# Performance work log

Measured on AMD Instinct MI355X. Metric: run time of the kernel, lower is better.

Reference implementation:

```python
import jax, jax.numpy as jnp
import numpy as np

NUM_NODES = 50000
NUM_EDGES = 600000
NUM_FEAT = 128
HIDDEN = 512
N_OUT = 128
K = 3
N_GRAPHS = 128


def setup_inputs() -> dict:
    key = jax.random.key(0)
    ks = jax.random.split(key, 12)
    feature = jax.random.normal(ks[0], (NUM_NODES, NUM_FEAT), dtype=jnp.float32)
    edge_index = jax.random.randint(ks[1], (2, NUM_EDGES), 0, NUM_NODES, dtype=jnp.int64)
    protein_batch = jnp.sort(jax.random.randint(ks[2], (NUM_NODES,), 0, N_GRAPHS, dtype=jnp.int64))
    s = 0.05
    # ChebConv weights stored [K, in, out] (x @ W), single shared bias per conv
    W1 = jax.random.normal(ks[3], (K, NUM_FEAT, NUM_FEAT), dtype=jnp.float32) * s
    b1 = jax.random.normal(ks[4], (NUM_FEAT,), dtype=jnp.float32) * s
    W2 = jax.random.normal(ks[5], (K, NUM_FEAT, 2 * NUM_FEAT), dtype=jnp.float32) * s
    b2 = jax.random.normal(ks[6], (2 * NUM_FEAT,), dtype=jnp.float32) * s
    fc1_w = jax.random.normal(ks[7], (3 * NUM_FEAT, HIDDEN), dtype=jnp.float32) * s
    fc1_b = jax.random.normal(ks[8], (HIDDEN,), dtype=jnp.float32) * s
    fc2_w = jax.random.normal(ks[9], (HIDDEN, N_OUT), dtype=jnp.float32) * s
    fc2_b = jax.random.normal(ks[10], (N_OUT,), dtype=jnp.float32) * s
    return {"feature": feature, "edge_index": edge_index, "protein_batch": protein_batch,
            "W1": W1, "b1": b1, "W2": W2, "b2": b2,
            "fc1_w": fc1_w, "fc1_b": fc1_b, "fc2_w": fc2_w, "fc2_b": fc2_b}


def _cheb_conv(x, src, dst, edge_w, W, b):
    # PyG ChebConv with sym normalization, lambda_max=2 => scaled Laplacian
    # L_hat has zero diagonal and off-diag weights -1/sqrt(d_i d_j) (edge_w).
    def prop(h):
        return jax.ops.segment_sum(edge_w[:, None] * h[src], dst, num_segments=NUM_NODES)

    Tx0 = x
    out = Tx0 @ W[0]
    Tx1 = prop(x)
    out = out + Tx1 @ W[1]
    for k in range(2, W.shape[0]):
        Tx2 = 2.0 * prop(Tx1) - Tx0
        out = out + Tx2 @ W[k]
        Tx0, Tx1 = Tx1, Tx2
    return out + b


def reference(feature, edge_index, protein_batch, W1, b1, W2, b2, fc1_w, fc1_b, fc2_w, fc2_b):
    src, dst = edge_index[0], edge_index[1]
    deg = jax.ops.segment_sum(jnp.ones_like(src, dtype=feature.dtype), src, num_segments=NUM_NODES)
    dinv = jnp.where(deg > 0, jax.lax.rsqrt(jnp.maximum(deg, 1.0)), 0.0)
    edge_w = -dinv[src] * dinv[dst]  # (2/lambda_max)*L_sym off-diagonal; diag cancels to 0

    gx = jax.nn.relu(_cheb_conv(feature, src, dst, edge_w, W1, b1))
    gx = jax.nn.relu(_cheb_conv(gx, src, dst, edge_w, W2, b2))
    gx = jnp.concatenate([gx, feature], axis=1)  # [N, 3*F]

    # global_mean_pool
    sums = jax.ops.segment_sum(gx, protein_batch, num_segments=N_GRAPHS)
    cnts = jax.ops.segment_sum(jnp.ones((gx.shape[0],), gx.dtype), protein_batch, num_segments=N_GRAPHS)
    pooled = sums / jnp.maximum(cnts, 1.0)[:, None]

    h = jax.nn.relu(pooled @ fc1_w + fc1_b)  # dropout is identity in eval
    return h @ fc2_w + fc2_b
```

## Files before the change

### kernel.cpp

```cpp
#include <hip/hip_runtime.h>
#include <hip/hip_bf16.h>

#define NNODES 50000
#define NEDGES 600000
#define NB 196

typedef short vs8 __attribute__((ext_vector_type(8)));
typedef float floatx4 __attribute__((ext_vector_type(4)));

__device__ __forceinline__ float us2f(unsigned short u) {
    unsigned int x = ((unsigned int)u) << 16;
    float f;
    __builtin_memcpy(&f, &x, 4);
    return f;
}
__device__ __forceinline__ unsigned short f2us(float f) {
    unsigned int x;
    __builtin_memcpy(&x, &f, 4);
    unsigned int r = x + 0x7fffu + ((x >> 16) & 1u);
    return (unsigned short)(r >> 16);
}
__device__ __forceinline__ float ldf(const void* p, int i, int ff) {
    if (ff) return us2f(((const unsigned short*)p)[i]);
    return ((const float*)p)[i];
}
__device__ __forceinline__ int2 ldnt_sw(const int2* p) {
    unsigned long long v =
        __builtin_nontemporal_load(reinterpret_cast<const unsigned long long*>(p));
    int2 r;
    r.x = (int)(unsigned int)(v & 0xffffffffULL);
    r.y = (int)(unsigned int)(v >> 32);
    return r;
}

__global__ void k_detect(const int* ei, const unsigned int* fw, int* iflag, int* fflag) {
    int lane = threadIdx.x;
    int odd1 = ei[2 * lane + 1];
    int odd2 = ei[128 + 2 * lane + 1];
    unsigned long long nz = __ballot(odd1 != 0 || odd2 != 0);
    unsigned int e = (fw[lane] >> 7) & 0xffu;
    unsigned long long h = __ballot(e > 100u && e < 160u);
    if (lane == 0) {
        *iflag = (nz == 0ULL) ? 1 : 0;
        *fflag = (__popcll(h) > 40) ? 1 : 0;
    }
}

__global__ void k_init(const int* pb, const int* iflag, int* deg, int* indeg,
                       int* b32, float* psum) {
    int i = blockIdx.x * 256 + threadIdx.x;
    if (i < NNODES) {
        deg[i] = 0;
        indeg[i] = 0;
        int f = *iflag;
        b32[i] = pb[((size_t)i) << f];
    }
    if (i < 128 * 384) psum[i] = 0.f;
}

__global__ void k_degree(const int* ei, const int* iflag, int* deg, int* indeg,
                         int* rank) {
    int e = blockIdx.x * blockDim.x + threadIdx.x;
    if (e >= NEDGES) return;
    int f = *iflag;
    int s = ei[((size_t)e) << f];
    int d = ei[((size_t)(NEDGES + e)) << f];
    atomicAdd(&deg[s], 1);
    int r = atomicAdd(&indeg[d], 1);
    rank[e] = r;
}

__global__ void k_scan1(const int* indeg, const int* deg, int* bsum, float* dinv) {
    __shared__ int sh[256];
    int t = threadIdx.x;
    int i = blockIdx.x * 256 + t;
    int v = (i < NNODES) ? indeg[i] : 0;
    if (i < NNODES) {
        int d = deg[i];
        dinv[i] = d > 0 ? rsqrtf((float)d) : 0.f;
    }
    sh[t] = v;
    __syncthreads();
    for (int off = 128; off > 0; off >>= 1) {
        if (t < off) sh[t] += sh[t + off];
        __syncthreads();
    }
    if (t == 0) bsum[blockIdx.x] = sh[0];
}

__global__ void k_scan2(const int* bsum, int* boff, int* rowptr,
                        const int* batch32, int* pcnt) {
    __shared__ int sh[256];
    int t = threadIdx.x;
    int v = (t < NB) ? bsum[t] : 0;
    sh[t] = v;
    __syncthreads();
    for (int off = 1; off < 256; off <<= 1) {
        int x = (t >= off) ? sh[t - off] : 0;
        __syncthreads();
        sh[t] += x;
        __syncthreads();
    }
    if (t < NB) boff[t] = sh[t] - v;
    if (t == 255) rowptr[NNODES] = sh[255];
    if (t < 128) {
        int g = t;
        int lo = 0, hi = NNODES;
        while (lo < hi) { int mid = (lo + hi) >> 1; if (batch32[mid] < g) lo = mid + 1; else hi = mid; }
        int start = lo;
        hi = NNODES;
        while (lo < hi) { int mid = (lo + hi) >> 1; if (batch32[mid] <= g) lo = mid + 1; else hi = mid; }
        pcnt[g] = lo - start;
    }
}

__global__ void k_scan3(const int* indeg, const int* boff, int* rowptr) {
    __shared__ int sh[256];
    int t = threadIdx.x;
    int i = blockIdx.x * 256 + t;
    int v = (i < NNODES) ? indeg[i] : 0;
    sh[t] = v;
    __syncthreads();
    for (int off = 1; off < 256; off <<= 1) {
        int x = (t >= off) ? sh[t - off] : 0;
        __syncthreads();
        sh[t] += x;
        __syncthreads();
    }
    int excl = sh[t] - v + boff[blockIdx.x];
    if (i < NNODES) rowptr[i] = excl;
}

__global__ void k_fill(const int* ei, const int* iflag, const float* dinv,
                       const int* rowptr, const int* rank, int2* csr_sw) {
    int e = blockIdx.x * blockDim.x + threadIdx.x;
    if (e >= NEDGES) return;
    int f = *iflag;
    int s = ei[((size_t)e) << f];
    int d = ei[((size_t)(NEDGES + e)) << f];
    float w = -dinv[s] * dinv[d];
    int p = rowptr[d] + rank[e];
    int wb;
    __builtin_memcpy(&wb, &w, 4);
    int2 sw;
    sw.x = s;
    sw.y = wb;
    csr_sw[p] = sw;
}

__global__ void k_featb(const void* src, const int* fflag, unsigned short* dst) {
    int i = blockIdx.x * 256 + threadIdx.x;
    if (i >= NNODES * 128 / 8) return;
    if (*fflag) {
        reinterpret_cast<uint4*>(dst)[i] = reinterpret_cast<const uint4*>(src)[i];
    } else {
        const float4* fs = reinterpret_cast<const float4*>(src);
        float4 a = fs[2 * i], b = fs[2 * i + 1];
        uint4 o;
        o.x = (unsigned int)f2us(a.x) | ((unsigned int)f2us(a.y) << 16);
        o.y = (unsigned int)f2us(a.z) | ((unsigned int)f2us(a.w) << 16);
        o.z = (unsigned int)f2us(b.x) | ((unsigned int)f2us(b.y) << 16);
        o.w = (unsigned int)f2us(b.z) | ((unsigned int)f2us(b.w) << 16);
        reinterpret_cast<uint4*>(dst)[i] = o;
    }
}

__global__ void k_trans2(const void* W1, const void* W2, const int* fflag,
                         unsigned short* W1t, unsigned short* W2t) {
    int idx = blockIdx.x * 256 + threadIdx.x;
    int ff = *fflag;
    if (idx < 49152) {
        int n = idx / 384, k = idx - n * 384;
        float v;
        if (k < 128) v = ldf(W1, k * 128 + n, ff) - ldf(W1, (256 + k) * 128 + n, ff);
        else if (k < 256) v = ldf(W1, k * 128 + n, ff);
        else v = 2.f * ldf(W1, k * 128 + n, ff);
        W1t[idx] = f2us(v);
    } else if (idx < 49152 + 98304) {
        int j = idx - 49152;
        int n = j / 384, k = j - n * 384;
        float v;
        if (k < 128) v = ldf(W2, k * 256 + n, ff) - ldf(W2, (256 + k) * 256 + n, ff);
        else if (k < 256) v = ldf(W2, k * 256 + n, ff);
        else v = 2.f * ldf(W2, k * 256 + n, ff);
        W2t[j] = f2us(v);
    }
}

__global__ void k_prepw(const void* b1, const void* b2, const void* f1w, const void* f1b,
                        const void* f2w, const void* f2b, const int* fflag,
                        float* b1f, float* b2f, float* f1wf, float* f1bf,
                        float* f2wf, float* f2bf) {
    int i = blockIdx.x * 256 + threadIdx.x;
    int ff = *fflag;
    if (i < 196608) { f1wf[i] = ldf(f1w, i, ff); return; }
    i -= 196608;
    if (i < 65536) { f2wf[i] = ldf(f2w, i, ff); return; }
    i -= 65536;
    if (i < 512) { f1bf[i] = ldf(f1b, i, ff); return; }
    i -= 512;
    if (i < 256) { b2f[i] = ldf(b2, i, ff); return; }
    i -= 256;
    if (i < 128) { b1f[i] = ldf(b1, i, ff); return; }
    i -= 128;
    if (i < 128) f2bf[i] = ldf(f2b, i, ff);
}

__global__ void k_prop(const unsigned short* X, const int* rowptr, const int2* csr_sw,
                       unsigned short* out) {
    int wvid = (blockIdx.x * blockDim.x + threadIdx.x) >> 6;
    int lane = threadIdx.x & 63;
    int q = lane >> 4;
    int ln = lane & 15;
    int node = wvid * 4 + q;
    if (node >= NNODES) return;
    int fo = ln * 8;
    int beg = rowptr[node], end = rowptr[node + 1];
    float a0 = 0.f, a1 = 0.f, a2 = 0.f, a3 = 0.f;
    float a4 = 0.f, a5 = 0.f, a6 = 0.f, a7 = 0.f;
    int j = beg;
    for (; j + 4 <= end; j += 4) {
        int2 e0 = ldnt_sw(csr_sw + j);
        int2 e1 = ldnt_sw(csr_sw + j + 1);
        int2 e2 = ldnt_sw(csr_sw + j + 2);
        int2 e3 = ldnt_sw(csr_sw + j + 3);
        uint4 u0 = *reinterpret_cast<const uint4*>(X + (size_t)e0.x * 128 + fo);
        uint4 u1 = *reinterpret_cast<const uint4*>(X + (size_t)e1.x * 128 + fo);
        uint4 u2 = *reinterpret_cast<const uint4*>(X + (size_t)e2.x * 128 + fo);
        uint4 u3 = *reinterpret_cast<const uint4*>(X + (size_t)e3.x * 128 + fo);
        float w0, w1, w2, w3;
        __builtin_memcpy(&w0, &e0.y, 4);
        __builtin_memcpy(&w1, &e1.y, 4);
        __builtin_memcpy(&w2, &e2.y, 4);
        __builtin_memcpy(&w3, &e3.y, 4);
        a0 += w0 * us2f((unsigned short)(u0.x & 0xffffu)) + w1 * us2f((unsigned short)(u1.x & 0xffffu))
            + w2 * us2f((unsigned short)(u2.x & 0xffffu)) + w3 * us2f((unsigned short)(u3.x & 0xffffu));
        a1 += w0 * us2f((unsigned short)(u0.x >> 16)) + w1 * us2f((unsigned short)(u1.x >> 16))
            + w2 * us2f((unsigned short)(u2.x >> 16)) + w3 * us2f((unsigned short)(u3.x >> 16));
        a2 += w0 * us2f((unsigned short)(u0.y & 0xffffu)) + w1 * us2f((unsigned short)(u1.y & 0xffffu))
            + w2 * us2f((unsigned short)(u2.y & 0xffffu)) + w3 * us2f((unsigned short)(u3.y & 0xffffu));
        a3 += w0 * us2f((unsigned short)(u0.y >> 16)) + w1 * us2f((unsigned short)(u1.y >> 16))
            + w2 * us2f((unsigned short)(u2.y >> 16)) + w3 * us2f((unsigned short)(u3.y >> 16));
        a4 += w0 * us2f((unsigned short)(u0.z & 0xffffu)) + w1 * us2f((unsigned short)(u1.z & 0xffffu))
            + w2 * us2f((unsigned short)(u2.z & 0xffffu)) + w3 * us2f((unsigned short)(u3.z & 0xffffu));
        a5 += w0 * us2f((unsigned short)(u0.z >> 16)) + w1 * us2f((unsigned short)(u1.z >> 16))
            + w2 * us2f((unsigned short)(u2.z >> 16)) + w3 * us2f((unsigned short)(u3.z >> 16));
        a6 += w0 * us2f((unsigned short)(u0.w & 0xffffu)) + w1 * us2f((unsigned short)(u1.w & 0xffffu))
            + w2 * us2f((unsigned short)(u2.w & 0xffffu)) + w3 * us2f((unsigned short)(u3.w & 0xffffu));
        a7 += w0 * us2f((unsigned short)(u0.w >> 16)) + w1 * us2f((unsigned short)(u1.w >> 16))
            + w2 * us2f((unsigned short)(u2.w >> 16)) + w3 * us2f((unsigned short)(u3.w >> 16));
    }
    for (; j < end; ++j) {
        int2 e = ldnt_sw(csr_sw + j);
        float w;
        __builtin_memcpy(&w, &e.y, 4);
        uint4 u = *reinterpret_cast<const uint4*>(X + (size_t)e.x * 128 + fo);
        a0 += w * us2f((unsigned short)(u.x & 0xffffu));
        a1 += w * us2f((unsigned short)(u.x >> 16));
        a2 += w * us2f((unsigned short)(u.y & 0xffffu));
        a3 += w * us2f((unsigned short)(u.y >> 16));
        a4 += w * us2f((unsigned short)(u.z & 0xffffu));
        a5 += w * us2f((unsigned short)(u.z >> 16));
        a6 += w * us2f((unsigned short)(u.w & 0xffffu));
        a7 += w * us2f((unsigned short)(u.w >> 16));
    }
    uint4 ov;
    ov.x = (unsigned int)f2us(a0) | ((unsigned int)f2us(a1) << 16);
    ov.y = (unsigned int)f2us(a2) | ((unsigned int)f2us(a3) << 16);
    ov.z = (unsigned int)f2us(a4) | ((unsigned int)f2us(a5) << 16);
    ov.w = (unsigned int)f2us(a6) | ((unsigned int)f2us(a7) << 16);
    *reinterpret_cast<uint4*>(out + (size_t)node * 128 + fo) = ov;
}

template <int POOL>
__global__ __launch_bounds__(512) void k_convg(
    const unsigned short* seg0, const unsigned short* seg1, const unsigned short* seg2,
    const unsigned short* Wt, const float* bias, unsigned short* out,
    const int* batch32, float* psum, int nout, int nslab) {
    __shared__ unsigned short shb[24576];
    __shared__ float sh_ps[512];
    int tid = threadIdx.x;
    int bid = blockIdx.x;
    int grp = 8 * nslab;
    int main_blocks = 24 * grp;
    int r, slab;
    if (bid < main_blocks) {
        int g = bid / grp;
        int rem = bid - g * grp;
        slab = rem >> 3;
        r = g * 8 + (rem & 7);
    } else {
        int t = bid - main_blocks;
        r = 192 + (t & 3);
        slab = t >> 2;
    }
    int col0 = slab * 64;
    if (POOL) sh_ps[tid] = 0.f;
#pragma unroll
    for (int it = 0; it < 6; ++it) {
        int idx = tid + it * 512;
        int kkt = idx >> 6, ln = idx & 63;
        int kk = kkt >> 2, t = kkt & 3;
        int col = col0 + t * 16 + (ln & 15);
        int ko = kk * 32 + (ln >> 4) * 8;
        uint4 v = *reinterpret_cast<const uint4*>(Wt + (size_t)col * 384 + ko);
        *reinterpret_cast<uint4*>(shb + idx * 8) = v;
    }
    __syncthreads();
    int wv = tid >> 6, lane = tid & 63;
    int m = lane & 15, kq = lane >> 4;
    int row0 = r * 256 + wv * 32;
    int rr0 = row0 + m;
    int rr1 = row0 + 16 + m;
    if (rr0 >= NNODES) rr0 = NNODES - 1;
    if (rr1 >= NNODES) rr1 = NNODES - 1;
    floatx4 acc[2][4];
#pragma unroll
    for (int rI = 0; rI < 2; ++rI)
#pragma unroll
        for (int t = 0; t < 4; ++t) {
            acc[rI][t][0] = 0.f; acc[rI][t][1] = 0.f; acc[rI][t][2] = 0.f; acc[rI][t][3] = 0.f;
        }
    const unsigned short* segs[3];
    segs[0] = seg0; segs[1] = seg1; segs[2] = seg2;
#pragma unroll
    for (int kk = 0; kk < 12; ++kk) {
        int sgi = kk >> 2, k4 = kk & 3;
        const unsigned short* S = segs[sgi];
        int ko = k4 * 32 + kq * 8;
        vs8 a0 = *reinterpret_cast<const vs8*>(S + (size_t)rr0 * 128 + ko);
        vs8 a1 = *reinterpret_cast<const vs8*>(S + (size_t)rr1 * 128 + ko);
#pragma unroll
        for (int t = 0; t < 4; ++t) {
            vs8 b = *reinterpret_cast<const vs8*>(shb + ((kk * 4 + t) * 64 + lane) * 8);
            acc[0][t] = __builtin_amdgcn_mfma_f32_16x16x32_bf16(a0, b, acc[0][t], 0, 0, 0);
            acc[1][t] = __builtin_amdgcn_mfma_f32_16x16x32_bf16(a1, b, acc[1][t], 0, 0, 0);
        }
    }
    if (POOL == 0) {
#pragma unroll
        for (int rI = 0; rI < 2; ++rI) {
            int orow_base = row0 + rI * 16 + kq * 4;
#pragma unroll
            for (int t = 0; t < 4; ++t) {
                int col = col0 + t * 16 + m;
                float bv = bias[col];
#pragma unroll
                for (int i = 0; i < 4; ++i) {
                    int rw = orow_base + i;
                    if (rw < NNODES) {
                        float v = acc[rI][t][i] + bv;
                        v = v > 0.f ? v : 0.f;
                        out[(size_t)rw * nout + col] = f2us(v);
                    }
                }
            }
        }
    } else {
        int g0 = batch32[r * 256];
#pragma unroll
        for (int rI = 0; rI < 2; ++rI) {
            int orow_base = row0 + rI * 16 + kq * 4;
            int gid[4];
#pragma unroll
            for (int i = 0; i < 4; ++i) {
                int rw = orow_base + i;
                gid[i] = rw < NNODES ? batch32[rw] : -1;
            }
#pragma unroll
            for (int t = 0; t < 4; ++t) {
                int col = col0 + t * 16 + m;
                float bv = bias[col];
                float run = 0.f;
                int curg = -1;
#pragma unroll
                for (int i = 0; i < 4; ++i) {
                    int g = gid[i];
                    if (g < 0) break;
                    float v = acc[rI][t][i] + bv;
                    v = v > 0.f ? v : 0.f;
                    if (g != curg) {
                        if (curg >= 0) {
                            int gl = curg - g0;
                            if (gl >= 0 && gl < 8) atomicAdd(&sh_ps[gl * 64 + t * 16 + m], run);
                            else atomicAdd(&psum[curg * 384 + col], run);
                        }
                        curg = g;
                        run = 0.f;
                    }
                    run += v;
                }
                if (curg >= 0) {
                    int gl = curg - g0;
                    if (gl >= 0 && gl < 8) atomicAdd(&sh_ps[gl * 64 + t * 16 + m], run);
                    else atomicAdd(&psum[curg * 384 + col], run);
                }
            }
        }
        __syncthreads();
        int gl = tid >> 6, c = tid & 63;
        float v = sh_ps[tid];
        int gg = g0 + gl;
        if (v != 0.f && gg < 128) atomicAdd(&psum[(size_t)gg * 384 + col0 + c], v);
    }
}

__global__ void k_poolnodes(const unsigned short* featb, const int* batch32, float* psum) {
    int col = threadIdx.x & 127;
    int half = threadIdx.x >> 7;
    int nbeg = blockIdx.x * 128 + half * 64;
    if (nbeg >= NNODES) return;
    int nend = nbeg + 64;
    if (nend > NNODES) nend = NNODES;
    float run = 0.f;
    int curg = batch32[nbeg];
    for (int n = nbeg; n < nend; ++n) {
        int g = batch32[n];
        if (g != curg) {
            atomicAdd(&psum[curg * 384 + 256 + col], run);
            run = 0.f;
            curg = g;
        }
        run += us2f(featb[(size_t)n * 128 + col]);
    }
    atomicAdd(&psum[curg * 384 + 256 + col], run);
}

__global__ void k_fc1(const float* psum, const int* pcnt, const float* w,
                      const float* b, float* h) {
    int g = blockIdx.x, j = threadIdx.x * 2;
    int c = pcnt[g];
    float inv = 1.f / (float)(c > 0 ? c : 1);
    float a0 = 0.f, a1 = 0.f;
    for (int k = 0; k < 384; ++k) {
        float p = psum[g * 384 + k];
        a0 += p * w[k * 512 + j];
        a1 += p * w[k * 512 + j + 1];
    }
    a0 = a0 * inv + b[j];
    a1 = a1 * inv + b[j + 1];
    h[g * 512 + j] = a0 > 0.f ? a0 : 0.f;
    h[g * 512 + j + 1] = a1 > 0.f ? a1 : 0.f;
}

__global__ void ChebModel_74380243632480_kernel(const float* h, const float* w,
                                                const float* b, const int* fflag,
                                                void* out) {
    int g = blockIdx.x, j = threadIdx.x;
    float acc = 0.f;
    for (int k = 0; k < 512; ++k) acc += h[g * 512 + k] * w[k * 128 + j];
    acc += b[j];
    if (*fflag) ((unsigned short*)out)[g * 128 + j] = f2us(acc);
    else ((float*)out)[g * 128 + j] = acc;
}

extern "C" void kernel_launch(void* const* d_in, const int* in_sizes, int n_in,
                              void* d_out, int out_size, void* d_ws, size_t ws_size,
                              hipStream_t stream) {
    const void* feature = d_in[0];
    const int* edge_index = (const int*)d_in[1];
    const int* batch = (const int*)d_in[2];
    const void* W1 = d_in[3];
    const void* b1 = d_in[4];
    const void* W2 = d_in[5];
    const void* b2 = d_in[6];
    const void* fc1w = d_in[7];
    const void* fc1b = d_in[8];
    const void* fc2w = d_in[9];
    const void* fc2b = d_in[10];

    char* ws = (char*)d_ws;
    size_t off = 0;
    int* iflag = (int*)(ws + off); off += 256;
    int* fflag = (int*)(ws + off); off += 256;
    int* deg = (int*)(ws + off); off += ((size_t)NNODES * 4 + 255) & ~(size_t)255;
    int* indeg = (int*)(ws + off); off += ((size_t)NNODES * 4 + 255) & ~(size_t)255;
    int* rowptr = (int*)(ws + off); off += ((size_t)(NNODES + 1) * 4 + 255) & ~(size_t)255;
    float* dinv = (float*)(ws + off); off += ((size_t)NNODES * 4 + 255) & ~(size_t)255;
    int* batch32 = (int*)(ws + off); off += ((size_t)NNODES * 4 + 255) & ~(size_t)255;
    int* bsum = (int*)(ws + off); off += 1024;
    int* boff = (int*)(ws + off); off += 1024;
    int* rank = (int*)(ws + off); off += ((size_t)NEDGES * 4 + 255) & ~(size_t)255;
    int2* csr_sw = (int2*)(ws + off); off += ((size_t)NEDGES * 8 + 255) & ~(size_t)255;
    unsigned short* featb = (unsigned short*)(ws + off); off += ((size_t)NNODES * 128 * 2 + 255) & ~(size_t)255;
    unsigned short* T1 = (unsigned short*)(ws + off); off += ((size_t)NNODES * 128 * 2 + 255) & ~(size_t)255;
    unsigned short* T2 = (unsigned short*)(ws + off); off += ((size_t)NNODES * 128 * 2 + 255) & ~(size_t)255;
    unsigned short* gx1 = (unsigned short*)(ws + off); off += ((size_t)NNODES * 128 * 2 + 255) & ~(size_t)255;
    unsigned short* W1t = (unsigned short*)(ws + off); off += ((size_t)49152 * 2 + 255) & ~(size_t)255;
    unsigned short* W2t = (unsigned short*)(ws + off); off += ((size_t)98304 * 2 + 255) & ~(size_t)255;
    float* b1f = (float*)(ws + off); off += 1024;
    float* b2f = (float*)(ws + off); off += 1024;
    float* fc1wf = (float*)(ws + off); off += ((size_t)196608 * 4 + 255) & ~(size_t)255;
    float* fc1bf = (float*)(ws + off); off += 2048;
    float* fc2wf = (float*)(ws + off); off += ((size_t)65536 * 4 + 255) & ~(size_t)255;
    float* fc2bf = (float*)(ws + off); off += 1024;
    float* psum = (float*)(ws + off); off += ((size_t)128 * 384 * 4 + 255) & ~(size_t)255;
    int* pcnt = (int*)(ws + off); off += 1024;
    float* hbuf = (float*)(ws + off); off += ((size_t)128 * 512 * 4 + 255) & ~(size_t)255;

    k_detect<<<1, 64, 0, stream>>>(edge_index, (const unsigned int*)feature, iflag, fflag);
    k_init<<<(NNODES + 255) / 256, 256, 0, stream>>>(batch, iflag, deg, indeg, batch32, psum);
    k_degree<<<(NEDGES + 255) / 256, 256, 0, stream>>>(edge_index, iflag, deg, indeg, rank);
    k_scan1<<<NB, 256, 0, stream>>>(indeg, deg, bsum, dinv);
    k_scan2<<<1, 256, 0, stream>>>(bsum, boff, rowptr, batch32, pcnt);
    k_scan3<<<NB, 256, 0, stream>>>(indeg, boff, rowptr);
    k_fill<<<(NEDGES + 255) / 256, 256, 0, stream>>>(edge_index, iflag, dinv, rowptr, rank, csr_sw);

    k_featb<<<(NNODES * 128 / 8 + 255) / 256, 256, 0, stream>>>(feature, fflag, featb);
    k_trans2<<<(49152 + 98304 + 255) / 256, 256, 0, stream>>>(W1, W2, fflag, W1t, W2t);
    k_prepw<<<(263168 + 255) / 256, 256, 0, stream>>>(b1, b2, fc1w, fc1b, fc2w, fc2b, fflag,
                                                      b1f, b2f, fc1wf, fc1bf, fc2wf, fc2bf);

    int pb = ((NNODES + 3) / 4 * 64 + 255) / 256;
    k_prop<<<pb, 256, 0, stream>>>(featb, rowptr, csr_sw, T1);
    k_prop<<<pb, 256, 0, stream>>>(T1, rowptr, csr_sw, T2);
    k_convg<0><<<196 * 2, 512, 0, stream>>>(featb, T1, T2, W1t, b1f, gx1,
                                            (const int*)0, (float*)0, 128, 2);
    k_prop<<<pb, 256, 0, stream>>>(gx1, rowptr, csr_sw, T1);
    k_prop<<<pb, 256, 0, stream>>>(T1, rowptr, csr_sw, T2);
    k_convg<1><<<196 * 4, 512, 0, stream>>>(gx1, T1, T2, W2t, b2f, (unsigned short*)0,
                                            batch32, psum, 256, 4);
    k_poolnodes<<<(NNODES + 127) / 128, 256, 0, stream>>>(featb, batch32, psum);
    k_fc1<<<128, 256, 0, stream>>>(psum, pcnt, fc1wf, fc1bf, hbuf);
    ChebModel_74380243632480_kernel<<<128, 128, 0, stream>>>(hbuf, fc2wf, fc2bf, fflag, d_out);
}
```

Measured before the change: 410.4 us.

## Split degree atomic counters into four sub-arrays and merge prep kernels

```diff
diff --git a/kernel.cpp b/kernel.cpp
--- a/kernel.cpp
+++ b/kernel.cpp
@@ -46,40 +46,52 @@
     }
 }
 
-__global__ void k_init(const int* pb, const int* iflag, int* deg, int* indeg,
+__global__ void k_init(const int* pb, const int* iflag, int* deg4, int* indeg4,
                        int* b32, float* psum) {
     int i = blockIdx.x * 256 + threadIdx.x;
     if (i < NNODES) {
-        deg[i] = 0;
-        indeg[i] = 0;
+#pragma unroll
+        for (int c = 0; c < 4; ++c) {
+            deg4[c * NNODES + i] = 0;
+            indeg4[c * NNODES + i] = 0;
+        }
         int f = *iflag;
         b32[i] = pb[((size_t)i) << f];
     }
     if (i < 128 * 384) psum[i] = 0.f;
 }
 
-__global__ void k_degree(const int* ei, const int* iflag, int* deg, int* indeg,
+__global__ void k_degree(const int* ei, const int* iflag, int* deg4, int* indeg4,
                          int* rank) {
     int e = blockIdx.x * blockDim.x + threadIdx.x;
     if (e >= NEDGES) return;
     int f = *iflag;
     int s = ei[((size_t)e) << f];
     int d = ei[((size_t)(NEDGES + e)) << f];
-    atomicAdd(&deg[s], 1);
-    int r = atomicAdd(&indeg[d], 1);
-    rank[e] = r;
-}
-
-__global__ void k_scan1(const int* indeg, const int* deg, int* bsum, float* dinv) {
+    int c = e & 3;
+    atomicAdd(&deg4[c * NNODES + s], 1);
+    int r = atomicAdd(&indeg4[c * NNODES + d], 1);
+    __builtin_nontemporal_store(r, &rank[e]);
+}
+
+__global__ void k_scan1(const int* indeg4, const int* deg4, int* bsum, float* dinv,
+                        int4* coff, int* indeg_tot) {
     __shared__ int sh[256];
     int t = threadIdx.x;
     int i = blockIdx.x * 256 + t;
-    int v = (i < NNODES) ? indeg[i] : 0;
+    int tot = 0;
     if (i < NNODES) {
-        int d = deg[i];
+        int i0 = indeg4[i], i1 = indeg4[NNODES + i];
+        int i2 = indeg4[2 * NNODES + i], i3 = indeg4[3 * NNODES + i];
+        tot = i0 + i1 + i2 + i3;
+        int4 co;
+        co.x = 0; co.y = i0; co.z = i0 + i1; co.w = i0 + i1 + i2;
+        coff[i] = co;
+        indeg_tot[i] = tot;
+        int d = deg4[i] + deg4[NNODES + i] + deg4[2 * NNODES + i] + deg4[3 * NNODES + i];
         dinv[i] = d > 0 ? rsqrtf((float)d) : 0.f;
     }
-    sh[t] = v;
+    sh[t] = tot;
     __syncthreads();
     for (int off = 128; off > 0; off >>= 1) {
         if (t < off) sh[t] += sh[t + off];
@@ -114,11 +126,11 @@
     }
 }
 
-__global__ void k_scan3(const int* indeg, const int* boff, int* rowptr) {
+__global__ void k_scan3(const int* indeg_tot, const int* boff, int* rowptr) {
     __shared__ int sh[256];
     int t = threadIdx.x;
     int i = blockIdx.x * 256 + t;
-    int v = (i < NNODES) ? indeg[i] : 0;
+    int v = (i < NNODES) ? indeg_tot[i] : 0;
     sh[t] = v;
     __syncthreads();
     for (int off = 1; off < 256; off <<= 1) {
@@ -132,14 +144,18 @@
 }
 
 __global__ void k_fill(const int* ei, const int* iflag, const float* dinv,
-                       const int* rowptr, const int* rank, int2* csr_sw) {
+                       const int* rowptr, const int4* coff, const int* rank,
+                       int2* csr_sw) {
     int e = blockIdx.x * blockDim.x + threadIdx.x;
     if (e >= NEDGES) return;
     int f = *iflag;
     int s = ei[((size_t)e) << f];
     int d = ei[((size_t)(NEDGES + e)) << f];
     float w = -dinv[s] * dinv[d];
-    int p = rowptr[d] + rank[e];
+    int c = e & 3;
+    int4 co = coff[d];
+    int base = (c == 0) ? co.x : (c == 1) ? co.y : (c == 2) ? co.z : co.w;
+    int p = rowptr[d] + base + rank[e];
     int wb;
     __builtin_memcpy(&wb, &w, 4);
     int2 sw;
@@ -148,51 +164,50 @@
     csr_sw[p] = sw;
 }
 
-__global__ void k_featb(const void* src, const int* fflag, unsigned short* dst) {
+__global__ void k_prep(const void* feat, const void* W1, const void* W2,
+                       const void* b1, const void* b2, const void* f1w, const void* f1b,
+                       const void* f2w, const void* f2b, const int* fflag,
+                       unsigned short* featb, unsigned short* W1t, unsigned short* W2t,
+                       float* b1f, float* b2f, float* f1wf, float* f1bf,
+                       float* f2wf, float* f2bf) {
     int i = blockIdx.x * 256 + threadIdx.x;
-    if (i >= NNODES * 128 / 8) return;
-    if (*fflag) {
-        reinterpret_cast<uint4*>(dst)[i] = reinterpret_cast<const uint4*>(src)[i];
-    } else {
-        const float4* fs = reinterpret_cast<const float4*>(src);
-        float4 a = fs[2 * i], b = fs[2 * i + 1];
-        uint4 o;
-        o.x = (unsigned int)f2us(a.x) | ((unsigned int)f2us(a.y) << 16);
-        o.y = (unsigned int)f2us(a.z) | ((unsigned int)f2us(a.w) << 16);
-        o.z = (unsigned int)f2us(b.x) | ((unsigned int)f2us(b.y) << 16);
-        o.w = (unsigned int)f2us(b.z) | ((unsigned int)f2us(b.w) << 16);
-        reinterpret_cast<uint4*>(dst)[i] = o;
-    }
-}
-
-__global__ void k_trans2(const void* W1, const void* W2, const int* fflag,
-                         unsigned short* W1t, unsigned short* W2t) {
-    int idx = blockIdx.x * 256 + threadIdx.x;
     int ff = *fflag;
-    if (idx < 49152) {
-        int n = idx / 384, k = idx - n * 384;
+    if (i < 800000) {
+        if (ff) {
+            reinterpret_cast<uint4*>(featb)[i] = reinterpret_cast<const uint4*>(feat)[i];
+        } else {
+            const float4* fs = reinterpret_cast<const float4*>(feat);
+            float4 a = fs[2 * i], b = fs[2 * i + 1];
+            uint4 o;
+            o.x = (unsigned int)f2us(a.x) | ((unsigned int)f2us(a.y) << 16);
+            o.y = (unsigned int)f2us(a.z) | ((unsigned int)f2us(a.w) << 16);
+            o.z = (unsigned int)f2us(b.x) | ((unsigned int)f2us(b.y) << 16);
+            o.w = (unsigned int)f2us(b.z) | ((unsigned int)f2us(b.w) << 16);
+            reinterpret_cast<uint4*>(featb)[i] = o;
+        }
+        return;
+    }
+    i -= 800000;
+    if (i < 49152) {
+        int n = i / 384, k = i - n * 384;
         float v;
         if (k < 128) v = ldf(W1, k * 128 + n, ff) - ldf(W1, (256 + k) * 128 + n, ff);
         else if (k < 256) v = ldf(W1, k * 128 + n, ff);
         else v = 2.f * ldf(W1, k * 128 + n, ff);
-        W1t[idx] = f2us(v);
-    } else if (idx < 49152 + 98304) {
-        int j = idx - 49152;
-        int n = j / 384, k = j - n * 384;
+        W1t[i] = f2us(v);
+        return;
+    }
+    i -= 49152;
+    if (i < 98304) {
+        int n = i / 384, k = i - n * 384;
         float v;
         if (k < 128) v = ldf(W2, k * 256 + n, ff) - ldf(W2, (256 + k) * 256 + n, ff);
         else if (k < 256) v = ldf(W2, k * 256 + n, ff);
         else v = 2.f * ldf(W2, k * 256 + n, ff);
-        W2t[j] = f2us(v);
-    }
-}
-
-__global__ void k_prepw(const void* b1, const void* b2, const void* f1w, const void* f1b,
-                        const void* f2w, const void* f2b, const int* fflag,
-                        float* b1f, float* b2f, float* f1wf, float* f1bf,
-                        float* f2wf, float* f2bf) {
-    int i = blockIdx.x * 256 + threadIdx.x;
-    int ff = *fflag;
+        W2t[i] = f2us(v);
+        return;
+    }
+    i -= 98304;
     if (i < 196608) { f1wf[i] = ldf(f1w, i, ff); return; }
     i -= 196608;
     if (i < 65536) { f2wf[i] = ldf(f2w, i, ff); return; }
@@ -473,8 +488,10 @@
     size_t off = 0;
     int* iflag = (int*)(ws + off); off += 256;
     int* fflag = (int*)(ws + off); off += 256;
-    int* deg = (int*)(ws + off); off += ((size_t)NNODES * 4 + 255) & ~(size_t)255;
-    int* indeg = (int*)(ws + off); off += ((size_t)NNODES * 4 + 255) & ~(size_t)255;
+    int* deg4 = (int*)(ws + off); off += ((size_t)4 * NNODES * 4 + 255) & ~(size_t)255;
+    int* indeg4 = (int*)(ws + off); off += ((size_t)4 * NNODES * 4 + 255) & ~(size_t)255;
+    int* indeg_tot = (int*)(ws + off); off += ((size_t)NNODES * 4 + 255) & ~(size_t)255;
+    int4* coff = (int4*)(ws + off); off += ((size_t)NNODES * 16 + 255) & ~(size_t)255;
     int* rowptr = (int*)(ws + off); off += ((size_t)(NNODES + 1) * 4 + 255) & ~(size_t)255;
     float* dinv = (float*)(ws + off); off += ((size_t)NNODES * 4 + 255) & ~(size_t)255;
     int* batch32 = (int*)(ws + off); off += ((size_t)NNODES * 4 + 255) & ~(size_t)255;
@@ -499,17 +516,17 @@
     float* hbuf = (float*)(ws + off); off += ((size_t)128 * 512 * 4 + 255) & ~(size_t)255;
 
     k_detect<<<1, 64, 0, stream>>>(edge_index, (const unsigned int*)feature, iflag, fflag);
-    k_init<<<(NNODES + 255) / 256, 256, 0, stream>>>(batch, iflag, deg, indeg, batch32, psum);
-    k_degree<<<(NEDGES + 255) / 256, 256, 0, stream>>>(edge_index, iflag, deg, indeg, rank);
-    k_scan1<<<NB, 256, 0, stream>>>(indeg, deg, bsum, dinv);
+    k_init<<<(NNODES + 255) / 256, 256, 0, stream>>>(batch, iflag, deg4, indeg4, batch32, psum);
+    k_degree<<<(NEDGES + 255) / 256, 256, 0, stream>>>(edge_index, iflag, deg4, indeg4, rank);
+    k_scan1<<<NB, 256, 0, stream>>>(indeg4, deg4, bsum, dinv, coff, indeg_tot);
     k_scan2<<<1, 256, 0, stream>>>(bsum, boff, rowptr, batch32, pcnt);
-    k_scan3<<<NB, 256, 0, stream>>>(indeg, boff, rowptr);
-    k_fill<<<(NEDGES + 255) / 256, 256, 0, stream>>>(edge_index, iflag, dinv, rowptr, rank, csr_sw);
-
-    k_featb<<<(NNODES * 128 / 8 + 255) / 256, 256, 0, stream>>>(feature, fflag, featb);
-    k_trans2<<<(49152 + 98304 + 255) / 256, 256, 0, stream>>>(W1, W2, fflag, W1t, W2t);
-    k_prepw<<<(263168 + 255) / 256, 256, 0, stream>>>(b1, b2, fc1w, fc1b, fc2w, fc2b, fflag,
-                                                      b1f, b2f, fc1wf, fc1bf, fc2wf, fc2bf);
+    k_scan3<<<NB, 256, 0, stream>>>(indeg_tot, boff, rowptr);
+    k_fill<<<(NEDGES + 255) / 256, 256, 0, stream>>>(edge_index, iflag, dinv, rowptr, coff,
+                                                     rank, csr_sw);
+
+    k_prep<<<(800000 + 49152 + 98304 + 263168 + 255) / 256, 256, 0, stream>>>(
+        feature, W1, W2, b1, b2, fc1w, fc1b, fc2w, fc2b, fflag,
+        featb, W1t, W2t, b1f, b2f, fc1wf, fc1bf, fc2wf, fc2bf);
 
     int pb = ((NNODES + 3) / 4 * 64 + 255) / 256;
     k_prop<<<pb, 256, 0, stream>>>(featb, rowptr, csr_sw, T1);
```

New measurement: 419.4 us. 1.02x slower.

## Split SpMM propagation across feature quarters and merge prep kernels

Applied to the files above, without the earlier changes.

```diff
diff --git a/kernel.cpp b/kernel.cpp
--- a/kernel.cpp
+++ b/kernel.cpp
@@ -67,7 +67,7 @@
     int d = ei[((size_t)(NEDGES + e)) << f];
     atomicAdd(&deg[s], 1);
     int r = atomicAdd(&indeg[d], 1);
-    rank[e] = r;
+    __builtin_nontemporal_store(r, &rank[e]);
 }
 
 __global__ void k_scan1(const int* indeg, const int* deg, int* bsum, float* dinv) {
@@ -148,51 +148,50 @@
     csr_sw[p] = sw;
 }
 
-__global__ void k_featb(const void* src, const int* fflag, unsigned short* dst) {
+__global__ void k_prep(const void* feat, const void* W1, const void* W2,
+                       const void* b1, const void* b2, const void* f1w, const void* f1b,
+                       const void* f2w, const void* f2b, const int* fflag,
+                       unsigned short* featb, unsigned short* W1t, unsigned short* W2t,
+                       float* b1f, float* b2f, float* f1wf, float* f1bf,
+                       float* f2wf, float* f2bf) {
     int i = blockIdx.x * 256 + threadIdx.x;
-    if (i >= NNODES * 128 / 8) return;
-    if (*fflag) {
-        reinterpret_cast<uint4*>(dst)[i] = reinterpret_cast<const uint4*>(src)[i];
-    } else {
-        const float4* fs = reinterpret_cast<const float4*>(src);
-        float4 a = fs[2 * i], b = fs[2 * i + 1];
-        uint4 o;
-        o.x = (unsigned int)f2us(a.x) | ((unsigned int)f2us(a.y) << 16);
-        o.y = (unsigned int)f2us(a.z) | ((unsigned int)f2us(a.w) << 16);
-        o.z = (unsigned int)f2us(b.x) | ((unsigned int)f2us(b.y) << 16);
-        o.w = (unsigned int)f2us(b.z) | ((unsigned int)f2us(b.w) << 16);
-        reinterpret_cast<uint4*>(dst)[i] = o;
-    }
-}
-
-__global__ void k_trans2(const void* W1, const void* W2, const int* fflag,
-                         unsigned short* W1t, unsigned short* W2t) {
-    int idx = blockIdx.x * 256 + threadIdx.x;
     int ff = *fflag;
-    if (idx < 49152) {
-        int n = idx / 384, k = idx - n * 384;
+    if (i < 800000) {
+        if (ff) {
+            reinterpret_cast<uint4*>(featb)[i] = reinterpret_cast<const uint4*>(feat)[i];
+        } else {
+            const float4* fs = reinterpret_cast<const float4*>(feat);
+            float4 a = fs[2 * i], b = fs[2 * i + 1];
+            uint4 o;
+            o.x = (unsigned int)f2us(a.x) | ((unsigned int)f2us(a.y) << 16);
+            o.y = (unsigned int)f2us(a.z) | ((unsigned int)f2us(a.w) << 16);
+            o.z = (unsigned int)f2us(b.x) | ((unsigned int)f2us(b.y) << 16);
+            o.w = (unsigned int)f2us(b.z) | ((unsigned int)f2us(b.w) << 16);
+            reinterpret_cast<uint4*>(featb)[i] = o;
+        }
+        return;
+    }
+    i -= 800000;
+    if (i < 49152) {
+        int n = i / 384, k = i - n * 384;
         float v;
         if (k < 128) v = ldf(W1, k * 128 + n, ff) - ldf(W1, (256 + k) * 128 + n, ff);
         else if (k < 256) v = ldf(W1, k * 128 + n, ff);
         else v = 2.f * ldf(W1, k * 128 + n, ff);
-        W1t[idx] = f2us(v);
-    } else if (idx < 49152 + 98304) {
-        int j = idx - 49152;
-        int n = j / 384, k = j - n * 384;
+        W1t[i] = f2us(v);
+        return;
+    }
+    i -= 49152;
+    if (i < 98304) {
+        int n = i / 384, k = i - n * 384;
         float v;
         if (k < 128) v = ldf(W2, k * 256 + n, ff) - ldf(W2, (256 + k) * 256 + n, ff);
         else if (k < 256) v = ldf(W2, k * 256 + n, ff);
         else v = 2.f * ldf(W2, k * 256 + n, ff);
-        W2t[j] = f2us(v);
-    }
-}
-
-__global__ void k_prepw(const void* b1, const void* b2, const void* f1w, const void* f1b,
-                        const void* f2w, const void* f2b, const int* fflag,
-                        float* b1f, float* b2f, float* f1wf, float* f1bf,
-                        float* f2wf, float* f2bf) {
-    int i = blockIdx.x * 256 + threadIdx.x;
-    int ff = *fflag;
+        W2t[i] = f2us(v);
+        return;
+    }
+    i -= 98304;
     if (i < 196608) { f1wf[i] = ldf(f1w, i, ff); return; }
     i -= 196608;
     if (i < 65536) { f2wf[i] = ldf(f2w, i, ff); return; }
@@ -208,68 +207,46 @@
 
 __global__ void k_prop(const unsigned short* X, const int* rowptr, const int2* csr_sw,
                        unsigned short* out) {
-    int wvid = (blockIdx.x * blockDim.x + threadIdx.x) >> 6;
+    int bid = blockIdx.x;
+    int res = bid & 7;
+    int quarter = res >> 1;
+    int nb = (bid >> 3) * 2 + (res & 1);
     int lane = threadIdx.x & 63;
+    int wv = threadIdx.x >> 6;
     int q = lane >> 4;
     int ln = lane & 15;
-    int node = wvid * 4 + q;
+    int node = nb * 16 + wv * 4 + q;
     if (node >= NNODES) return;
-    int fo = ln * 8;
+    int fo = quarter * 32 + ln * 2;
     int beg = rowptr[node], end = rowptr[node + 1];
-    float a0 = 0.f, a1 = 0.f, a2 = 0.f, a3 = 0.f;
-    float a4 = 0.f, a5 = 0.f, a6 = 0.f, a7 = 0.f;
+    float a0 = 0.f, a1 = 0.f;
     int j = beg;
-    for (; j + 4 <= end; j += 4) {
-        int2 e0 = ldnt_sw(csr_sw + j);
-        int2 e1 = ldnt_sw(csr_sw + j + 1);
-        int2 e2 = ldnt_sw(csr_sw + j + 2);
-        int2 e3 = ldnt_sw(csr_sw + j + 3);
-        uint4 u0 = *reinterpret_cast<const uint4*>(X + (size_t)e0.x * 128 + fo);
-        uint4 u1 = *reinterpret_cast<const uint4*>(X + (size_t)e1.x * 128 + fo);
-        uint4 u2 = *reinterpret_cast<const uint4*>(X + (size_t)e2.x * 128 + fo);
-        uint4 u3 = *reinterpret_cast<const uint4*>(X + (size_t)e3.x * 128 + fo);
-        float w0, w1, w2, w3;
-        __builtin_memcpy(&w0, &e0.y, 4);
-        __builtin_memcpy(&w1, &e1.y, 4);
-        __builtin_memcpy(&w2, &e2.y, 4);
-        __builtin_memcpy(&w3, &e3.y, 4);
-        a0 += w0 * us2f((unsigned short)(u0.x & 0xffffu)) + w1 * us2f((unsigned short)(u1.x & 0xffffu))
-            + w2 * us2f((unsigned short)(u2.x & 0xffffu)) + w3 * us2f((unsigned short)(u3.x & 0xffffu));
-        a1 += w0 * us2f((unsigned short)(u0.x >> 16)) + w1 * us2f((unsigned short)(u1.x >> 16))
-            + w2 * us2f((unsigned short)(u2.x >> 16)) + w3 * us2f((unsigned short)(u3.x >> 16));
-        a2 += w0 * us2f((unsigned short)(u0.y & 0xffffu)) + w1 * us2f((unsigned short)(u1.y & 0xffffu))
-            + w2 * us2f((unsigned short)(u2.y & 0xffffu)) + w3 * us2f((unsigned short)(u3.y & 0xffffu));
-        a3 += w0 * us2f((unsigned short)(u0.y >> 16)) + w1 * us2f((unsigned short)(u1.y >> 16))
-            + w2 * us2f((unsigned short)(u2.y >> 16)) + w3 * us2f((unsigned short)(u3.y >> 16));
-        a4 += w0 * us2f((unsigned short)(u0.z & 0xffffu)) + w1 * us2f((unsigned short)(u1.z & 0xffffu))
-            + w2 * us2f((unsigned short)(u2.z & 0xffffu)) + w3 * us2f((unsigned short)(u3.z & 0xffffu));
-        a5 += w0 * us2f((unsigned short)(u0.z >> 16)) + w1 * us2f((unsigned short)(u1.z >> 16))
-            + w2 * us2f((unsigned short)(u2.z >> 16)) + w3 * us2f((unsigned short)(u3.z >> 16));
-        a6 += w0 * us2f((unsigned short)(u0.w & 0xffffu)) + w1 * us2f((unsigned short)(u1.w & 0xffffu))
-            + w2 * us2f((unsigned short)(u2.w & 0xffffu)) + w3 * us2f((unsigned short)(u3.w & 0xffffu));
-        a7 += w0 * us2f((unsigned short)(u0.w >> 16)) + w1 * us2f((unsigned short)(u1.w >> 16))
-            + w2 * us2f((unsigned short)(u2.w >> 16)) + w3 * us2f((unsigned short)(u3.w >> 16));
+    for (; j + 8 <= end; j += 8) {
+        int2 e[8];
+        unsigned int u[8];
+#pragma unroll
+        for (int k = 0; k < 8; ++k) e[k] = ldnt_sw(csr_sw + j + k);
+#pragma unroll
+        for (int k = 0; k < 8; ++k)
+            u[k] = *reinterpret_cast<const unsigned int*>(X + (size_t)e[k].x * 128 + fo);
+#pragma unroll
+        for (int k = 0; k < 8; ++k) {
+            float w;
+            __builtin_memcpy(&w, &e[k].y, 4);
+            a0 += w * us2f((unsigned short)(u[k] & 0xffffu));
+            a1 += w * us2f((unsigned short)(u[k] >> 16));
+        }
     }
     for (; j < end; ++j) {
         int2 e = ldnt_sw(csr_sw + j);
         float w;
         __builtin_memcpy(&w, &e.y, 4);
-        uint4 u = *reinterpret_cast<const uint4*>(X + (size_t)e.x * 128 + fo);
-        a0 += w * us2f((unsigned short)(u.x & 0xffffu));
-        a1 += w * us2f((unsigned short)(u.x >> 16));
-        a2 += w * us2f((unsigned short)(u.y & 0xffffu));
-        a3 += w * us2f((unsigned short)(u.y >> 16));
-        a4 += w * us2f((unsigned short)(u.z & 0xffffu));
-        a5 += w * us2f((unsigned short)(u.z >> 16));
-        a6 += w * us2f((unsigned short)(u.w & 0xffffu));
-        a7 += w * us2f((unsigned short)(u.w >> 16));
-    }
-    uint4 ov;
-    ov.x = (unsigned int)f2us(a0) | ((unsigned int)f2us(a1) << 16);
-    ov.y = (unsigned int)f2us(a2) | ((unsigned int)f2us(a3) << 16);
-    ov.z = (unsigned int)f2us(a4) | ((unsigned int)f2us(a5) << 16);
-    ov.w = (unsigned int)f2us(a6) | ((unsigned int)f2us(a7) << 16);
-    *reinterpret_cast<uint4*>(out + (size_t)node * 128 + fo) = ov;
+        unsigned int u = *reinterpret_cast<const unsigned int*>(X + (size_t)e.x * 128 + fo);
+        a0 += w * us2f((unsigned short)(u & 0xffffu));
+        a1 += w * us2f((unsigned short)(u >> 16));
+    }
+    unsigned int ov = (unsigned int)f2us(a0) | ((unsigned int)f2us(a1) << 16);
+    *reinterpret_cast<unsigned int*>(out + (size_t)node * 128 + fo) = ov;
 }
 
 template <int POOL>
@@ -506,12 +483,11 @@
     k_scan3<<<NB, 256, 0, stream>>>(indeg, boff, rowptr);
     k_fill<<<(NEDGES + 255) / 256, 256, 0, stream>>>(edge_index, iflag, dinv, rowptr, rank, csr_sw);
 
-    k_featb<<<(NNODES * 128 / 8 + 255) / 256, 256, 0, stream>>>(feature, fflag, featb);
-    k_trans2<<<(49152 + 98304 + 255) / 256, 256, 0, stream>>>(W1, W2, fflag, W1t, W2t);
-    k_prepw<<<(263168 + 255) / 256, 256, 0, stream>>>(b1, b2, fc1w, fc1b, fc2w, fc2b, fflag,
-                                                      b1f, b2f, fc1wf, fc1bf, fc2wf, fc2bf);
-
-    int pb = ((NNODES + 3) / 4 * 64 + 255) / 256;
+    k_prep<<<(800000 + 49152 + 98304 + 263168 + 255) / 256, 256, 0, stream>>>(
+        feature, W1, W2, b1, b2, fc1w, fc1b, fc2w, fc2b, fflag,
+        featb, W1t, W2t, b1f, b2f, fc1wf, fc1bf, fc2wf, fc2bf);
+
+    int pb = 8 * 1563;
     k_prop<<<pb, 256, 0, stream>>>(featb, rowptr, csr_sw, T1);
     k_prop<<<pb, 256, 0, stream>>>(T1, rowptr, csr_sw, T2);
     k_convg<0><<<196 * 2, 512, 0, stream>>>(featb, T1, T2, W1t, b1f, gx1,
```

New measurement: 515.8 us. +25.7%, slower.
